# Optimization experiments

Hardware: AMD Instinct MI355X
Metric: run time of the kernel (lower is better)

Reference implementation:

```python
import jax, jax.numpy as jnp
import numpy as np


def setup_inputs() -> dict:
    key = jax.random.key(0)
    k1, k2 = jax.random.split(key)
    B, C, H, W = 8, 64, 32, 32
    K = 8192
    x = jax.random.normal(k1, (B, C, H, W), dtype=jnp.float32)
    codebook = jax.random.normal(k2, (K, C), dtype=jnp.float32)
    return {"x": x, "codebook": codebook}


def reference(x, codebook):
    """Faithful JAX version of VQVAE.quantize().

    x:        [B, C, H, W] latent (output of pre_quant_conv)
    codebook: [K, C] embedding weight
    Returns (quant_out [B,C,H,W], commitment_loss, codebook_loss, indices [B,H,W]).
    """
    B, C, H, W = x.shape
    # [B, H, W, C] -> [B, N, C]
    xf = jnp.transpose(x, (0, 2, 3, 1)).reshape(B, H * W, C)

    # Squared pairwise distances (argmin of cdist == argmin of squared dist).
    x2 = jnp.sum(xf * xf, axis=-1, keepdims=True)            # [B, N, 1]
    e2 = jnp.sum(codebook * codebook, axis=-1)               # [K]
    xe = jnp.einsum('bnc,kc->bnk', xf, codebook)             # [B, N, K]
    d2 = x2 + e2[None, None, :] - 2.0 * xe                   # [B, N, K]
    idx = jnp.argmin(d2, axis=-1)                            # [B, N]

    quant = codebook[idx.reshape(-1)]                        # [B*N, C]
    xflat = xf.reshape(-1, C)                                # [B*N, C]

    commitment_loss = jnp.mean((jax.lax.stop_gradient(quant) - xflat) ** 2)
    codebook_loss = jnp.mean((quant - jax.lax.stop_gradient(xflat)) ** 2)

    # Straight-through estimator.
    quant_st = xflat + jax.lax.stop_gradient(quant - xflat)
    quant_out = jnp.transpose(quant_st.reshape(B, H, W, C), (0, 3, 1, 2))
    indices = idx.reshape(B, H, W)
    return quant_out, commitment_loss, codebook_loss, indices
```

## Files before the change

kernel.cpp:

```cpp
#include <hip/hip_runtime.h>


#define N_PTS   8192
#define K_CODES 8192
#define C_DIM   64
#define HWSZ    1024
#define QOUT_N  524288
#define SPLITS  32
#define NCH     4

#define WS_PACK  0
#define WS_CBS   2097152
#define WS_E2H   4194304
#define WS_PART  4227072

typedef __attribute__((ext_vector_type(8))) short    short8;
typedef __attribute__((ext_vector_type(8))) _Float16 half8;
typedef __attribute__((ext_vector_type(4))) float    floatx4;

__device__ __forceinline__ half8 as_h8(short8 v) {
    return __builtin_bit_cast(half8, v);
}
__device__ __forceinline__ void split2(float v, unsigned short& h,
                                       unsigned short& m) {
    _Float16 hh = (_Float16)v;
    float r = v - (float)hh;
    _Float16 mm = (_Float16)r;
    h = __builtin_bit_cast(unsigned short, hh);
    m = __builtin_bit_cast(unsigned short, mm);
}

__global__ __launch_bounds__(256)
void vq_prep_kernel(const float* __restrict__ cb,
                    unsigned short* __restrict__ cbS,
                    float* __restrict__ e2h)
{
    const int k = blockIdx.x * 256 + threadIdx.x;
    const float* row = cb + k * C_DIM;
    float s = 0.0f;
    #pragma unroll
    for (int g = 0; g < 8; ++g) {
        float4 a = *(const float4*)(row + g * 8);
        float4 b = *(const float4*)(row + g * 8 + 4);
        float vv[8] = {a.x, a.y, a.z, a.w, b.x, b.y, b.z, b.w};
        unsigned short h8[8], m8[8];
        #pragma unroll
        for (int j = 0; j < 8; ++j) {
            s = fmaf(vv[j], vv[j], s);
            split2(vv[j], h8[j], m8[j]);
        }
        *(uint4*)(cbS + ((size_t)(0 * 8 + g) * 8192 + k) * 8) = *(const uint4*)h8;
        *(uint4*)(cbS + ((size_t)(1 * 8 + g) * 8192 + k) * 8) = *(const uint4*)m8;
    }
    e2h[k] = 0.5f * s;
}

__global__ __launch_bounds__(256, 4)
void vq_argmin_kernel(const float* __restrict__ x,
                      const unsigned short* __restrict__ cbS,
                      const float* __restrict__ e2h,
                      unsigned long long* __restrict__ packedS)
{
    const int tid   = threadIdx.x;
    const int lane  = tid & 63;
    const int w     = tid >> 6;
    const int col   = lane & 15;
    const int quad  = lane >> 4;
    const int mb    = blockIdx.x;
    const int split = blockIdx.y;
    const int m0    = mb * 128 + w * 32;
    const int nb0   = split * 256;

    const int bimg = m0 >> 10;
    const int hw0  = m0 & 1023;
    const float* xb = x + (size_t)bimg * (C_DIM * HWSZ);
    half8 af[2][2][2];
    #pragma unroll
    for (int t = 0; t < 2; ++t) {
        const int hw = hw0 + t * 16 + col;
        #pragma unroll
        for (int s = 0; s < 2; ++s) {
            unsigned short h8[8], m8[8];
            #pragma unroll
            for (int j = 0; j < 8; ++j) {
                float v = xb[(size_t)(s * 32 + quad * 8 + j) * HWSZ + hw];
                split2(v, h8[j], m8[j]);
            }
            af[t][0][s] = as_h8(*(const short8*)h8);
            af[t][1][s] = as_h8(*(const short8*)m8);
        }
    }

    float bestv[2][4];
    int   besti[2][4];
    #pragma unroll
    for (int t = 0; t < 2; ++t)
        #pragma unroll
        for (int r = 0; r < 4; ++r) {
            bestv[t][r] = __uint_as_float(0xFF800000u);
            besti[t][r] = 0;
        }

    #pragma clang loop unroll(disable)
    for (int ch = 0; ch < NCH; ++ch) {
        const int k0 = nb0 + ch * 64;
        #pragma unroll
        for (int tl = 0; tl < 4; ++tl) {
            const int code = k0 + tl * 16 + col;
            half8 bf[2][2];
            #pragma unroll
            for (int p = 0; p < 2; ++p)
                #pragma unroll
                for (int s = 0; s < 2; ++s) {
                    int seg = p * 8 + s * 4 + quad;
                    bf[p][s] = as_h8(*(const short8*)(cbS + ((size_t)seg * 8192 + code) * 8));
                }
            float me2 = -e2h[code];

            floatx4 acc[2];
            #pragma unroll
            for (int t = 0; t < 2; ++t) acc[t] = (floatx4){me2, me2, me2, me2};

            #pragma unroll
            for (int s = 0; s < 2; ++s) {
                #pragma unroll
                for (int t = 0; t < 2; ++t)
                    acc[t] = __builtin_amdgcn_mfma_f32_16x16x32_f16(af[t][0][s], bf[0][s], acc[t], 0, 0, 0);
                #pragma unroll
                for (int t = 0; t < 2; ++t)
                    acc[t] = __builtin_amdgcn_mfma_f32_16x16x32_f16(af[t][0][s], bf[1][s], acc[t], 0, 0, 0);
                #pragma unroll
                for (int t = 0; t < 2; ++t)
                    acc[t] = __builtin_amdgcn_mfma_f32_16x16x32_f16(af[t][1][s], bf[0][s], acc[t], 0, 0, 0);
            }

            #pragma unroll
            for (int t = 0; t < 2; ++t)
                #pragma unroll
                for (int r = 0; r < 4; ++r) {
                    float sc = acc[t][r];
                    bool gt = sc > bestv[t][r];
                    bestv[t][r] = gt ? sc   : bestv[t][r];
                    besti[t][r] = gt ? code : besti[t][r];
                }
        }
    }

    unsigned long long own = 0;
    #pragma unroll
    for (int t = 0; t < 2; ++t)
        #pragma unroll
        for (int r = 0; r < 4; ++r) {
            unsigned u = __float_as_uint(-bestv[t][r]);
            u = ((int)u < 0) ? ~u : (u | 0x80000000u);
            unsigned long long p = ((unsigned long long)u << 32) | (unsigned)besti[t][r];
            #pragma unroll
            for (int msk = 1; msk < 16; msk <<= 1) {
                unsigned long long q = __shfl_xor(p, msk, 64);
                p = (q < p) ? q : p;
            }
            own = (col == t * 4 + r) ? p : own;
        }
    if (col < 8) {
        const int mpt = m0 + (col >> 2) * 16 + quad * 4 + (col & 3);
        packedS[(size_t)split * N_PTS + mpt] = own;
    }
}

__global__ __launch_bounds__(256)
void vq_gather_kernel(const float* __restrict__ x,
                      const float* __restrict__ cb,
                      const unsigned long long* __restrict__ packedS,
                      float* __restrict__ out,
                      float* __restrict__ part)
{
    __shared__ unsigned long long sred[8][32];
    const int tid = threadIdx.x;
    const int p   = tid & 31;
    const int sg  = tid >> 5;
    const int n0  = blockIdx.x * 32;
    const int n   = n0 + p;

    {
        unsigned long long v = packedS[(size_t)(sg * 4) * N_PTS + n];
        #pragma unroll
        for (int j = 1; j < 4; ++j) {
            unsigned long long q = packedS[(size_t)(sg * 4 + j) * N_PTS + n];
            v = (q < v) ? q : v;
        }
        sred[sg][p] = v;
    }
    __syncthreads();

    unsigned long long v = sred[0][p];
    #pragma unroll
    for (int s = 1; s < 8; ++s) {
        unsigned long long q = sred[s][p];
        v = (q < v) ? q : v;
    }
    const int idx = (int)(v & 0xFFFFFFFFull);
    if (tid < 32) out[QOUT_N + 2 + n0 + tid] = (float)idx;

    const int c0  = sg * 8;
    const int b   = n >> 10;
    const int hw  = n & 1023;
    const float* xb = x   + (size_t)b * (C_DIM * HWSZ) + hw;
    float*       ob = out + (size_t)b * (C_DIM * HWSZ) + hw;

    float s = 0.0f;
    #pragma unroll
    for (int c4 = 0; c4 < 2; ++c4) {
        float4 q = *(const float4*)(cb + (size_t)idx * C_DIM + c0 + c4 * 4);
        float qa[4] = {q.x, q.y, q.z, q.w};
        #pragma unroll
        for (int j = 0; j < 4; ++j) {
            int c = c0 + c4 * 4 + j;
            float xv = xb[c * HWSZ];
            float d  = qa[j] - xv;
            s = fmaf(d, d, s);
            ob[c * HWSZ] = xv + d;
        }
    }

    #pragma unroll
    for (int off = 32; off > 0; off >>= 1) s += __shfl_down(s, off, 64);
    if ((tid & 63) == 0) part[blockIdx.x * 4 + (tid >> 6)] = s;
}

__global__ __launch_bounds__(256)
void vq_final_kernel(const float* __restrict__ part, float* __restrict__ out)
{
    __shared__ float w[4];
    float s = part[threadIdx.x] + part[threadIdx.x + 256]
            + part[threadIdx.x + 512] + part[threadIdx.x + 768];
    #pragma unroll
    for (int off = 32; off > 0; off >>= 1) s += __shfl_down(s, off, 64);
    if ((threadIdx.x & 63) == 0) w[threadIdx.x >> 6] = s;
    __syncthreads();
    if (threadIdx.x == 0) {
        float m = (w[0] + w[1] + w[2] + w[3]) * (1.0f / (float)QOUT_N);
        out[QOUT_N]     = m;
        out[QOUT_N + 1] = m;
    }
}

extern "C" void kernel_launch(void* const* d_in, const int* in_sizes, int n_in,
                              void* d_out, int out_size, void* d_ws, size_t ws_size,
                              hipStream_t stream)
{
    const float* x  = (const float*)d_in[0];
    const float* cb = (const float*)d_in[1];
    float* out = (float*)d_out;
    char*  ws  = (char*)d_ws;
    (void)ws_size;

    unsigned long long* packedS = (unsigned long long*)(ws + WS_PACK);
    unsigned short* cbS = (unsigned short*)(ws + WS_CBS);
    float* e2h = (float*)(ws + WS_E2H);
    float* part = (float*)(ws + WS_PART);

    vq_prep_kernel<<<32, 256, 0, stream>>>(cb, cbS, e2h);
    vq_argmin_kernel<<<dim3(64, SPLITS), 256, 0, stream>>>(x, cbS, e2h, packedS);
    vq_gather_kernel<<<256, 256, 0, stream>>>(x, cb, packedS, out, part);
    vq_final_kernel<<<1, 256, 0, stream>>>(part, out);
}
```

Before: 98.28 us.

## Parallelize codebook prep per row-segment and fuse final loss reduction via ticket

The prep kernel now uses eight threads per codebook row, one per 8-channel group, reducing the squared norm with shuffles. This launches 256 blocks instead of 32 and fills more of the GPU. The separate final-reduction kernel is removed: the last gather block to finish, found with an atomic ticket counter that the prep kernel resets, sums the partials and writes both losses. This saves one kernel launch but adds a fence and an atomic to every gather block.

```diff
diff --git a/kernel.cpp b/kernel.cpp
--- a/kernel.cpp
+++ b/kernel.cpp
@@ -13,6 +13,7 @@
 #define WS_CBS   2097152
 #define WS_E2H   4194304
 #define WS_PART  4227072
+#define WS_TICK  4231168
 
 typedef __attribute__((ext_vector_type(8))) short    short8;
 typedef __attribute__((ext_vector_type(8))) _Float16 half8;
@@ -33,26 +34,31 @@
 __global__ __launch_bounds__(256)
 void vq_prep_kernel(const float* __restrict__ cb,
                     unsigned short* __restrict__ cbS,
-                    float* __restrict__ e2h)
-{
-    const int k = blockIdx.x * 256 + threadIdx.x;
-    const float* row = cb + k * C_DIM;
+                    float* __restrict__ e2h,
+                    int* __restrict__ ticket)
+{
+    const int gt = blockIdx.x * 256 + threadIdx.x;
+    const int k  = gt >> 3;
+    const int g  = gt & 7;
+    if (gt == 0) *ticket = 0;
+
+    const float* rp = cb + (size_t)k * C_DIM + g * 8;
+    float4 a = *(const float4*)(rp);
+    float4 b = *(const float4*)(rp + 4);
+    float vv[8] = {a.x, a.y, a.z, a.w, b.x, b.y, b.z, b.w};
+    unsigned short h8[8], m8[8];
     float s = 0.0f;
     #pragma unroll
-    for (int g = 0; g < 8; ++g) {
-        float4 a = *(const float4*)(row + g * 8);
-        float4 b = *(const float4*)(row + g * 8 + 4);
-        float vv[8] = {a.x, a.y, a.z, a.w, b.x, b.y, b.z, b.w};
-        unsigned short h8[8], m8[8];
-        #pragma unroll
-        for (int j = 0; j < 8; ++j) {
-            s = fmaf(vv[j], vv[j], s);
-            split2(vv[j], h8[j], m8[j]);
-        }
-        *(uint4*)(cbS + ((size_t)(0 * 8 + g) * 8192 + k) * 8) = *(const uint4*)h8;
-        *(uint4*)(cbS + ((size_t)(1 * 8 + g) * 8192 + k) * 8) = *(const uint4*)m8;
-    }
-    e2h[k] = 0.5f * s;
+    for (int j = 0; j < 8; ++j) {
+        s = fmaf(vv[j], vv[j], s);
+        split2(vv[j], h8[j], m8[j]);
+    }
+    *(uint4*)(cbS + ((size_t)(0 * 8 + g) * 8192 + k) * 8) = *(const uint4*)h8;
+    *(uint4*)(cbS + ((size_t)(1 * 8 + g) * 8192 + k) * 8) = *(const uint4*)m8;
+
+    #pragma unroll
+    for (int msk = 1; msk < 8; msk <<= 1) s += __shfl_xor(s, msk, 64);
+    if (g == 0) e2h[k] = 0.5f * s;
 }
 
 __global__ __launch_bounds__(256, 4)
@@ -172,9 +178,12 @@
                       const float* __restrict__ cb,
                       const unsigned long long* __restrict__ packedS,
                       float* __restrict__ out,
-                      float* __restrict__ part)
+                      float* __restrict__ part,
+                      int* __restrict__ ticket)
 {
     __shared__ unsigned long long sred[8][32];
+    __shared__ float wloss[4];
+    __shared__ int lastFlag;
     const int tid = threadIdx.x;
     const int p   = tid & 31;
     const int sg  = tid >> 5;
@@ -225,22 +234,28 @@
     #pragma unroll
     for (int off = 32; off > 0; off >>= 1) s += __shfl_down(s, off, 64);
     if ((tid & 63) == 0) part[blockIdx.x * 4 + (tid >> 6)] = s;
-}
-
-__global__ __launch_bounds__(256)
-void vq_final_kernel(const float* __restrict__ part, float* __restrict__ out)
-{
-    __shared__ float w[4];
-    float s = part[threadIdx.x] + part[threadIdx.x + 256]
-            + part[threadIdx.x + 512] + part[threadIdx.x + 768];
-    #pragma unroll
-    for (int off = 32; off > 0; off >>= 1) s += __shfl_down(s, off, 64);
-    if ((threadIdx.x & 63) == 0) w[threadIdx.x >> 6] = s;
+
     __syncthreads();
-    if (threadIdx.x == 0) {
-        float m = (w[0] + w[1] + w[2] + w[3]) * (1.0f / (float)QOUT_N);
-        out[QOUT_N]     = m;
-        out[QOUT_N + 1] = m;
+    if (tid == 0) {
+        __threadfence();
+        int prev = atomicAdd(ticket, 1);
+        lastFlag = (prev == 255);
+    }
+    __syncthreads();
+    if (lastFlag) {
+        __threadfence();
+        float s2 = part[tid] + part[tid + 256]
+                 + part[tid + 512] + part[tid + 768];
+        #pragma unroll
+        for (int off = 32; off > 0; off >>= 1) s2 += __shfl_down(s2, off, 64);
+        if ((tid & 63) == 0) wloss[tid >> 6] = s2;
+        __syncthreads();
+        if (tid == 0) {
+            float m = (wloss[0] + wloss[1] + wloss[2] + wloss[3])
+                    * (1.0f / (float)QOUT_N);
+            out[QOUT_N]     = m;
+            out[QOUT_N + 1] = m;
+        }
     }
 }
 
@@ -258,9 +273,9 @@
     unsigned short* cbS = (unsigned short*)(ws + WS_CBS);
     float* e2h = (float*)(ws + WS_E2H);
     float* part = (float*)(ws + WS_PART);
-
-    vq_prep_kernel<<<32, 256, 0, stream>>>(cb, cbS, e2h);
+    int* ticket = (int*)(ws + WS_TICK);
+
+    vq_prep_kernel<<<256, 256, 0, stream>>>(cb, cbS, e2h, ticket);
     vq_argmin_kernel<<<dim3(64, SPLITS), 256, 0, stream>>>(x, cbS, e2h, packedS);
-    vq_gather_kernel<<<256, 256, 0, stream>>>(x, cb, packedS, out, part);
-    vq_final_kernel<<<1, 256, 0, stream>>>(part, out);
-}
+    vq_gather_kernel<<<256, 256, 0, stream>>>(x, cb, packedS, out, part, ticket);
+}
```

Result: slower. 101.9 us (+3.7%).
